# Performance work log

Hardware: AMD Instinct MI355X
Metric: run time of the kernel (lower is better)

## Reference

```python
import jax, jax.numpy as jnp
import numpy as np
import math

B, LQ, LK, D = 8, 4096, 32768, 64
LKS = min(8000, LK)                                    # sampled key window (K[:, :8000])
UPART = min(5 * LQ * int(np.ceil(np.log1p(LKS))), LKS)  # = 8000


def setup_inputs() -> dict:
    key = jax.random.key(0)
    k1, k2, k3, k4 = jax.random.split(key, 4)
    q = jax.random.normal(k1, (B, LQ, D), dtype=jnp.float32)
    K = jax.random.normal(k2, (B, LK, D), dtype=jnp.float32)
    V = jax.random.normal(k3, (B, LK, D), dtype=jnp.float32)
    index_sample = jax.random.randint(k4, (UPART,), 0, LKS)  # torch.randint(0, L_K, (U_part,))
    return {"q": q, "K": K, "V": V, "index_sample": index_sample}


def reference(q, K, V, index_sample):
    L_K = min(8000, K.shape[1])            # K_sample = K[:, :8000]; L_K = K_sample.size(1)
    L_Q = q.shape[1]
    d_k = q.shape[-1]
    log_L_Q = int(np.ceil(np.log1p(L_Q)))
    u = min(5 * log_L_Q, L_Q)

    # gather sampled keys (indices < 8000, indexing full K as in the source)
    K_samp = K[:, index_sample, :]                         # [B, U_part, D]
    QKs = jnp.einsum('bqd,bud->bqu', q, K_samp)            # [B, L_Q, U_part]
    # sparsity measure: max - mean (divided by L_K as in torch.div(sum, L_K))
    M = QKs.max(axis=-1) - QKs.sum(axis=-1) / L_K          # [B, L_Q]
    # torch topk(largest=False) -> smallest u values of M
    _, M_top = jax.lax.top_k(-M, u)                        # [B, u]
    Q_reduce = jnp.take_along_axis(q, M_top[:, :, None], axis=1)  # [B, u, D]

    attn_scores = jnp.einsum('bud,bkd->buk', Q_reduce, K) / math.sqrt(d_k)  # [B, u, L_K_full]
    attn_probs = jax.nn.softmax(attn_scores, axis=-1)
    attn_output = jnp.einsum('buk,bkd->bud', attn_probs, V)                  # [B, u, D]
    return attn_output, attn_scores
```

## Files before the change

kernel.cpp:

```cpp
#include <hip/hip_runtime.h>

#define BB 8
#define LQ 4096
#define LK 32768
#define DD 64
#define UU 8000
#define NU 45
#define TQ2 128
#define TUC 160
#define NCH (UU/TUC)
#define CHB (TUC*DD*2)
#define KT5 512
#define NT5 64

typedef short short8 __attribute__((ext_vector_type(8)));
typedef float floatx16 __attribute__((ext_vector_type(16)));

__device__ __forceinline__ float bf2f(unsigned short h){ return __uint_as_float(((unsigned int)h) << 16); }
__device__ __forceinline__ unsigned short f2bf(float f){
  unsigned int u = __float_as_uint(f);
  u += 0x7FFFu + ((u >> 16) & 1u);
  return (unsigned short)(u >> 16);
}
__device__ __forceinline__ unsigned int fkey(float v){
  unsigned int u = __float_as_uint(v);
  return (u & 0x80000000u) ? ~u : (u | 0x80000000u);
}

__global__ __launch_bounds__(256) void k_gather(const float* __restrict__ Kg, const int* __restrict__ idx,
                                                unsigned short* __restrict__ khi, unsigned short* __restrict__ kmid){
  const int b = blockIdx.y;
  const int row = blockIdx.x*32 + (threadIdx.x >> 3);
  const int oct = threadIdx.x & 7;
  const float* src = Kg + ((size_t)(b*LK + idx[row]))*DD + oct*8;
  float x[8];
  #pragma unroll
  for (int j=0;j<8;j++) x[j] = src[j];
  unsigned short h[8], m[8];
  #pragma unroll
  for (int j=0;j<8;j++){
    h[j] = f2bf(x[j]);
    m[j] = f2bf(x[j] - bf2f(h[j]));
  }
  const int osl = oct ^ (row & 7);
  size_t o = ((size_t)(b*UU + row))*DD + osl*8;
  #pragma unroll
  for (int j=0;j<8;j++){ khi[o+j]=h[j]; kmid[o+j]=m[j]; }
}

__global__ __launch_bounds__(64) void k_spart(const float* __restrict__ Kg, const int* __restrict__ idx,
                                              float* __restrict__ Spart){
  const int g = blockIdx.x, b = blockIdx.y, d = threadIdx.x;
  float acc = 0.0f;
  for (int j=0;j<64;j++){
    int u = g*64 + j;
    acc += Kg[((size_t)(b*LK + idx[u]))*DD + d];
  }
  Spart[((size_t)(b*125 + g))*DD + d] = acc;
}
__global__ __launch_bounds__(64) void k_sred(const float* __restrict__ Spart, float* __restrict__ Sb){
  const int b = blockIdx.x, d = threadIdx.x;
  float acc = 0.0f;
  for (int g=0; g<125; g++) acc += Spart[((size_t)(b*125 + g))*DD + d];
  Sb[b*DD + d] = acc;
}

__device__ __forceinline__ void stage_chunk(const char* gh, const char* gm,
                                            unsigned short* Bhb, unsigned short* Bmb,
                                            int w, int lane){
  #pragma unroll
  for (int i=0;i<5;i++){
    const int u = w*5 + i;
    if (u < 20){
      __builtin_amdgcn_global_load_lds(
        (const __attribute__((address_space(1))) void*)(gh + u*1024 + lane*16),
        (__attribute__((address_space(3))) void*)((char*)Bhb + u*1024 + lane*16),
        16, 0, 0);
    } else {
      __builtin_amdgcn_global_load_lds(
        (const __attribute__((address_space(1))) void*)(gm + (u-20)*1024 + lane*16),
        (__attribute__((address_space(3))) void*)((char*)Bmb + (u-20)*1024 + lane*16),
        16, 0, 0);
    }
  }
}

__global__ __launch_bounds__(512,2) void k_Mm(const float* __restrict__ q,
                                              const unsigned short* __restrict__ khi,
                                              const unsigned short* __restrict__ kmid,
                                              float* __restrict__ amaxG, int* __restrict__ acargG){
  const int wg = blockIdx.x;
  const int b = wg & 7, qt = wg >> 3;
  const int tid = threadIdx.x;
  const int w = tid >> 6, lane = tid & 63;
  const int tr = w & 3, sp = w >> 2;
  const int l31 = lane & 31, lh = lane >> 5;
  __shared__ __align__(16) unsigned short Bh[2][TUC*DD];
  __shared__ __align__(16) unsigned short Bm[2][TUC*DD];
  __shared__ float combV[TQ2][2];
  __shared__ int   combC[TQ2][2];

  const int qrow = qt*TQ2 + tr*32 + l31;
  short8 ahi[4], amid[4];
  {
    const float* qp = q + ((size_t)(b*LQ) + qrow)*DD;
    #pragma unroll
    for (int s=0;s<4;s++){
      const int d0 = s*16 + lh*8;
      float4 x0 = *(const float4*)(qp + d0);
      float4 x1 = *(const float4*)(qp + d0 + 4);
      float xs[8] = {x0.x,x0.y,x0.z,x0.w,x1.x,x1.y,x1.z,x1.w};
      short8 h, m;
      #pragma unroll
      for (int j=0;j<8;j++){
        unsigned short hb = f2bf(xs[j]);
        unsigned short mb = f2bf(xs[j] - bf2f(hb));
        h[j] = (short)hb; m[j] = (short)mb;
      }
      ahi[s]=h; amid[s]=m;
    }
  }

  float vmax[16]; int carg[16];
  #pragma unroll
  for (int r=0;r<16;r++){ vmax[r]=-INFINITY; carg[r]=0; }

  const size_t kbyte = (size_t)b*UU*DD*2;
  const char* ghbase = (const char*)khi + kbyte;
  const char* gmbase = (const char*)kmid + kbyte;

  stage_chunk(ghbase, gmbase, &Bh[0][0], &Bm[0][0], w, lane);
  int cur = 0;

  for (int c=0;c<NCH;c++){
    __syncthreads();
    if (c+1 < NCH){
      stage_chunk(ghbase + (size_t)(c+1)*CHB, gmbase + (size_t)(c+1)*CHB,
                  &Bh[cur^1][0], &Bm[cur^1][0], w, lane);
    }
    float lmax[16];
    #pragma unroll
    for (int r=0;r<16;r++) lmax[r] = -INFINITY;
    for (int t = ((c ^ sp) & 1); t < 5; t += 2){
      floatx16 accA = {0.f,0.f,0.f,0.f,0.f,0.f,0.f,0.f,0.f,0.f,0.f,0.f,0.f,0.f,0.f,0.f};
      floatx16 accB = {0.f,0.f,0.f,0.f,0.f,0.f,0.f,0.f,0.f,0.f,0.f,0.f,0.f,0.f,0.f,0.f};
      #pragma unroll
      for (int s=0;s<4;s++){
        const int eo = (t*32 + l31)*DD + (((s*2 + lh) ^ (l31 & 7))*8);
        short8 bh = *(const short8*)(&Bh[cur][eo]);
        short8 bm = *(const short8*)(&Bm[cur][eo]);
        if (s & 1){
          accB = __builtin_amdgcn_mfma_f32_32x32x16_bf16(amid[s], bh, accB, 0, 0, 0);
          accB = __builtin_amdgcn_mfma_f32_32x32x16_bf16(ahi[s],  bm, accB, 0, 0, 0);
          accB = __builtin_amdgcn_mfma_f32_32x32x16_bf16(ahi[s],  bh, accB, 0, 0, 0);
        } else {
          accA = __builtin_amdgcn_mfma_f32_32x32x16_bf16(amid[s], bh, accA, 0, 0, 0);
          accA = __builtin_amdgcn_mfma_f32_32x32x16_bf16(ahi[s],  bm, accA, 0, 0, 0);
          accA = __builtin_amdgcn_mfma_f32_32x32x16_bf16(ahi[s],  bh, accA, 0, 0, 0);
        }
      }
      #pragma unroll
      for (int r=0;r<16;r++) lmax[r] = fmaxf(lmax[r], accA[r] + accB[r]);
    }
    #pragma unroll
    for (int r=0;r<16;r++){
      if (lmax[r] > vmax[r]){ vmax[r] = lmax[r]; carg[r] = c; }
    }
    cur ^= 1;
  }
  #pragma unroll
  for (int st=1; st<32; st<<=1){
    #pragma unroll
    for (int r=0;r<16;r++){
      float ov = __shfl_xor(vmax[r], st);
      int   oc = __shfl_xor(carg[r], st);
      if (ov > vmax[r]){ vmax[r]=ov; carg[r]=oc; }
    }
  }
  if (l31 == 0){
    #pragma unroll
    for (int r=0;r<16;r++){
      int m = (r&3) + 8*(r>>2) + 4*lh;
      int ql = tr*32 + m;
      combV[ql][sp] = vmax[r];
      combC[ql][sp] = carg[r];
    }
  }
  __syncthreads();
  if (tid < TQ2){
    float v0 = combV[tid][0], v1 = combV[tid][1];
    int   c0 = combC[tid][0], c1 = combC[tid][1];
    bool t1 = v1 > v0;
    amaxG[(size_t)b*LQ + qt*TQ2 + tid] = t1 ? v1 : v0;
    acargG[(size_t)b*LQ + qt*TQ2 + tid] = t1 ? c1 : c0;
  }
}

__global__ __launch_bounds__(256) void k_bucket(const int* __restrict__ acargG,
                                                int* __restrict__ qlist, int* __restrict__ bstart){
  const int b = blockIdx.x, tid = threadIdx.x;
  __shared__ int cnt[NCH];
  __shared__ int pos[NCH];
  if (tid < NCH) cnt[tid] = 0;
  __syncthreads();
  for (int qq = tid; qq < LQ; qq += 256){
    int ch = acargG[(size_t)b*LQ + qq];
    ch = (ch < 0) ? 0 : ((ch >= NCH) ? NCH-1 : ch);
    atomicAdd(&cnt[ch], 1);
  }
  __syncthreads();
  if (tid == 0){
    int acc = 0;
    for (int c=0;c<NCH;c++){ pos[c] = acc; bstart[b*64 + c] = acc; acc += cnt[c]; }
    bstart[b*64 + NCH] = acc;
  }
  __syncthreads();
  for (int qq = tid; qq < LQ; qq += 256){
    int ch = acargG[(size_t)b*LQ + qq];
    ch = (ch < 0) ? 0 : ((ch >= NCH) ? NCH-1 : ch);
    int p = atomicAdd(&pos[ch], 1);
    p = (p < 0) ? 0 : ((p >= LQ) ? LQ-1 : p);
    qlist[(size_t)b*LQ + p] = qq;
  }
}

__global__ __launch_bounds__(256,3) void k_refb(const float* __restrict__ q, const float* __restrict__ Kg,
                                                const int* __restrict__ idx, const float* __restrict__ Sb,
                                                const int* __restrict__ qlist, const int* __restrict__ bstart,
                                                float* __restrict__ M){
  const int wg = blockIdx.x;
  const int b = wg & 7;
  const int r0 = wg >> 3;
  const int ch = r0 >> 2, part = r0 & 3;
  const int tid = threadIdx.x;
  const int w = tid >> 6, lane = tid & 63;
  const int quad = lane & 3, rg = lane >> 2;
  __shared__ __align__(16) float Kl[TUC*DD];
  float4* Kl4 = (float4*)Kl;
  for (int g = tid; g < TUC*16; g += 256){
    int row = g >> 4, s = g & 15;
    int gidx = idx[ch*TUC + row];
    float4 v = *(const float4*)(Kg + ((size_t)(b*LK + gidx))*DD + s*4);
    Kl4[row*16 + (s ^ (row & 7))] = v;
  }
  __syncthreads();

  const float4* sp4 = (const float4*)(Sb + b*DD + quad*16);
  const float4 S0 = sp4[0], S1 = sp4[1], S2 = sp4[2], S3 = sp4[3];
  const int sl0 = ((quad<<2)|0) ^ (rg & 7);
  const int sl1 = ((quad<<2)|1) ^ (rg & 7);
  const int sl2 = ((quad<<2)|2) ^ (rg & 7);
  const int sl3 = ((quad<<2)|3) ^ (rg & 7);
  const int rbs = rg*16;
  const int s0 = bstart[b*64 + ch], s1 = bstart[b*64 + ch + 1];
  const int gw = part*4 + w;

  for (int i = s0 + (gw<<1); i < s1; i += 32){
    const int qa = qlist[(size_t)b*LQ + i];
    const int i2 = (i+1 < s1) ? i+1 : i;
    const int qb = qlist[(size_t)b*LQ + i2];
    const float4* ap = (const float4*)(q + ((size_t)(b*LQ + qa))*DD + quad*16);
    const float4* bp = (const float4*)(q + ((size_t)(b*LQ + qb))*DD + quad*16);
    const float4 A0 = ap[0], A1 = ap[1], A2 = ap[2], A3 = ap[3];
    const float4 B0 = bp[0], B1 = bp[1], B2 = bp[2], B3 = bp[3];
    float mxa = -INFINITY, mxb = -INFINITY;
    #pragma unroll
    for (int p=0;p<10;p++){
      const int base = p*256 + rbs;
      float4 k0 = Kl4[base + sl0];
      float4 k1 = Kl4[base + sl1];
      float4 k2 = Kl4[base + sl2];
      float4 k3 = Kl4[base + sl3];
      float a0 = A0.x*k0.x, a1 = A0.y*k0.y, a2 = A0.z*k0.z, a3 = A0.w*k0.w;
      a0 = fmaf(A1.x,k1.x,a0); a1 = fmaf(A1.y,k1.y,a1); a2 = fmaf(A1.z,k1.z,a2); a3 = fmaf(A1.w,k1.w,a3);
      a0 = fmaf(A2.x,k2.x,a0); a1 = fmaf(A2.y,k2.y,a1); a2 = fmaf(A2.z,k2.z,a2); a3 = fmaf(A2.w,k2.w,a3);
      a0 = fmaf(A3.x,k3.x,a0); a1 = fmaf(A3.y,k3.y,a1); a2 = fmaf(A3.z,k3.z,a2); a3 = fmaf(A3.w,k3.w,a3);
      float c0 = B0.x*k0.x, c1 = B0.y*k0.y, c2 = B0.z*k0.z, c3 = B0.w*k0.w;
      c0 = fmaf(B1.x,k1.x,c0); c1 = fmaf(B1.y,k1.y,c1); c2 = fmaf(B1.z,k1.z,c2); c3 = fmaf(B1.w,k1.w,c3);
      c0 = fmaf(B2.x,k2.x,c0); c1 = fmaf(B2.y,k2.y,c1); c2 = fmaf(B2.z,k2.z,c2); c3 = fmaf(B2.w,k2.w,c3);
      c0 = fmaf(B3.x,k3.x,c0); c1 = fmaf(B3.y,k3.y,c1); c2 = fmaf(B3.z,k3.z,c2); c3 = fmaf(B3.w,k3.w,c3);
      float sa = (a0+a1)+(a2+a3);
      float sc = (c0+c1)+(c2+c3);
      sa += __shfl_xor(sa, 1);
      sa += __shfl_xor(sa, 2);
      sc += __shfl_xor(sc, 1);
      sc += __shfl_xor(sc, 2);
      mxa = fmaxf(mxa, sa);
      mxb = fmaxf(mxb, sc);
    }
    #pragma unroll
    for (int st=4; st<64; st<<=1){
      mxa = fmaxf(mxa, __shfl_xor(mxa, st));
      mxb = fmaxf(mxb, __shfl_xor(mxb, st));
    }
    float m0 = A0.x*S0.x, m1 = A0.y*S0.y, m2 = A0.z*S0.z, m3 = A0.w*S0.w;
    m0 = fmaf(A1.x,S1.x,m0); m1 = fmaf(A1.y,S1.y,m1); m2 = fmaf(A1.z,S1.z,m2); m3 = fmaf(A1.w,S1.w,m3);
    m0 = fmaf(A2.x,S2.x,m0); m1 = fmaf(A2.y,S2.y,m1); m2 = fmaf(A2.z,S2.z,m2); m3 = fmaf(A2.w,S2.w,m3);
    m0 = fmaf(A3.x,S3.x,m0); m1 = fmaf(A3.y,S3.y,m1); m2 = fmaf(A3.z,S3.z,m2); m3 = fmaf(A3.w,S3.w,m3);
    float msa = (m0+m1)+(m2+m3);
    msa += __shfl_xor(msa, 1);
    msa += __shfl_xor(msa, 2);
    float n0 = B0.x*S0.x, n1 = B0.y*S0.y, n2 = B0.z*S0.z, n3 = B0.w*S0.w;
    n0 = fmaf(B1.x,S1.x,n0); n1 = fmaf(B1.y,S1.y,n1); n2 = fmaf(B1.z,S1.z,n2); n3 = fmaf(B1.w,S1.w,n3);
    n0 = fmaf(B2.x,S2.x,n0); n1 = fmaf(B2.y,S2.y,n1); n2 = fmaf(B2.z,S2.z,n2); n3 = fmaf(B2.w,S2.w,n3);
    n0 = fmaf(B3.x,S3.x,n0); n1 = fmaf(B3.y,S3.y,n1); n2 = fmaf(B3.z,S3.z,n2); n3 = fmaf(B3.w,S3.w,n3);
    float msb = (n0+n1)+(n2+n3);
    msb += __shfl_xor(msb, 1);
    msb += __shfl_xor(msb, 2);
    if (lane == 0){
      M[(size_t)b*LQ + qa] = mxa - msa * (1.0f/8000.0f);
      if (i2 != i) M[(size_t)b*LQ + qb] = mxb - msb * (1.0f/8000.0f);
    }
  }
}

__global__ __launch_bounds__(256) void k_select(const float* __restrict__ Mg,
                                                const float* __restrict__ q,
                                                int* __restrict__ MtopG, float* __restrict__ Qred){
  const int b = blockIdx.x, tid = threadIdx.x;
  __shared__ float Mv[LQ];
  __shared__ unsigned long long wmin[4];
  __shared__ int mtop[NU];
  __shared__ int selB;
  for (int qq = tid; qq < LQ; qq += 256) Mv[qq] = Mg[(size_t)b*LQ + qq];
  __syncthreads();
  unsigned long long lm = ~0ull;
  #pragma unroll
  for (int i=0;i<16;i++){
    int qq = tid + 256*i;
    unsigned long long kk = (((unsigned long long)fkey(Mv[qq]))<<32) | (unsigned int)qq;
    lm = (kk < lm) ? kk : lm;
  }
  for (int i=0;i<NU;i++){
    unsigned long long v = lm;
    #pragma unroll
    for (int st=1; st<64; st<<=1){
      unsigned long long o = __shfl_xor(v, st);
      v = (o < v) ? o : v;
    }
    if ((tid & 63) == 0) wmin[tid>>6] = v;
    __syncthreads();
    if (tid == 0){
      unsigned long long g01 = (wmin[0] < wmin[1]) ? wmin[0] : wmin[1];
      unsigned long long g23 = (wmin[2] < wmin[3]) ? wmin[2] : wmin[3];
      unsigned long long g = (g01 < g23) ? g01 : g23;
      int sel = (int)(g & 0xFFFFFFFFull);
      mtop[i] = sel; selB = sel; Mv[sel] = INFINITY;
    }
    __syncthreads();
    int sel = selB;
    if (tid == (sel & 255)){
      unsigned long long nl = ~0ull;
      #pragma unroll
      for (int j=0;j<16;j++){
        int qq = tid + 256*j;
        unsigned long long kk = (((unsigned long long)fkey(Mv[qq]))<<32) | (unsigned int)qq;
        nl = (kk < nl) ? kk : nl;
      }
      lm = nl;
    }
    __syncthreads();
  }
  if (tid < NU) MtopG[b*NU + tid] = mtop[tid];
  for (int e = tid; e < NU*DD; e += 256){
    int ui = e >> 6, d = e & 63;
    Qred[((size_t)(b*NU + ui))*DD + d] = q[((size_t)(b*LQ + mtop[ui]))*DD + d];
  }
}

#define QFMA(i) { float4 p = qr4[i]; \
  a0 = fmaf(kv##i.x, p.x, a0); a1 = fmaf(kv##i.y, p.y, a1); \
  a2 = fmaf(kv##i.z, p.z, a2); a3 = fmaf(kv##i.w, p.w, a3); }

__global__ __launch_bounds__(256) void k_scores(const float* __restrict__ Kg,
                                                const float* __restrict__ Qred,
                                                float* __restrict__ out1,
                                                float* __restrict__ pm, float* __restrict__ pl){
  const int b = blockIdx.y;
  const int k = blockIdx.x*256 + threadIdx.x;
  const int lane = threadIdx.x & 63, w = threadIdx.x >> 6;
  const int pi = blockIdx.x*4 + w;
  const float4* kp4 = (const float4*)(Kg + ((size_t)(b*LK + k))*DD);
  const float4 kv0  = kp4[0],  kv1  = kp4[1],  kv2  = kp4[2],  kv3  = kp4[3];
  const float4 kv4  = kp4[4],  kv5  = kp4[5],  kv6  = kp4[6],  kv7  = kp4[7];
  const float4 kv8  = kp4[8],  kv9  = kp4[9],  kv10 = kp4[10], kv11 = kp4[11];
  const float4 kv12 = kp4[12], kv13 = kp4[13], kv14 = kp4[14], kv15 = kp4[15];
  for (int u=0; u<NU; u++){
    const float4* qr4 = (const float4*)(Qred + ((size_t)(b*NU+u))*DD);
    float a0 = 0.f, a1 = 0.f, a2 = 0.f, a3 = 0.f;
    QFMA(0)  QFMA(1)  QFMA(2)  QFMA(3)
    QFMA(4)  QFMA(5)  QFMA(6)  QFMA(7)
    QFMA(8)  QFMA(9)  QFMA(10) QFMA(11)
    QFMA(12) QFMA(13) QFMA(14) QFMA(15)
    float s = ((a0+a1)+(a2+a3)) * 0.125f;
    out1[((size_t)(b*NU+u)<<15) + k] = s;
    float mw = s;
    #pragma unroll
    for (int st=1; st<64; st<<=1) mw = fmaxf(mw, __shfl_xor(mw, st));
    float e = __expf(s - mw);
    #pragma unroll
    for (int st=1; st<64; st<<=1) e += __shfl_xor(e, st);
    if (lane == 0){
      size_t r = (size_t)(b*NU + u);
      pm[r*512 + pi] = mw;
      pl[r*512 + pi] = e;
    }
  }
}

__global__ __launch_bounds__(256) void k_rowred(const float* __restrict__ pm, const float* __restrict__ pl,
                                                float* __restrict__ rowm, float* __restrict__ rowinvl){
  const int r = blockIdx.x, tid = threadIdx.x;
  __shared__ float red[256];
  float m = -INFINITY;
  for (int i = tid; i < 512; i += 256) m = fmaxf(m, pm[(size_t)r*512 + i]);
  red[tid] = m; __syncthreads();
  for (int s=128;s>0;s>>=1){ if (tid<s) red[tid] = fmaxf(red[tid], red[tid+s]); __syncthreads(); }
  m = red[0]; __syncthreads();
  float sm = 0.0f;
  for (int i = tid; i < 512; i += 256)
    sm += pl[(size_t)r*512 + i] * __expf(pm[(size_t)r*512 + i] - m);
  red[tid] = sm; __syncthreads();
  for (int s=128;s>0;s>>=1){ if (tid<s) red[tid] += red[tid+s]; __syncthreads(); }
  if (tid==0){ rowm[r] = m; rowinvl[r] = 1.0f/red[0]; }
}

__global__ __launch_bounds__(512) void k_pv(const float* __restrict__ Vg,
                                            const float* __restrict__ out1,
                                            const float* __restrict__ rowm, const float* __restrict__ rowinvl,
                                            float* __restrict__ pvpart){
  const int kt = blockIdx.x, b = blockIdx.y, tid = threadIdx.x;
  const int lane = tid & 63, w = tid >> 6;
  const int u0 = w*6;
  __shared__ float Vl[128][65];
  __shared__ __align__(16) float Pl[48][132];
  float acc[6];
  #pragma unroll
  for (int j=0;j<6;j++) acc[j] = 0.0f;
  for (int sc=0; sc<4; sc++){
    const int k0 = kt*KT5 + sc*128;
    {
      int r = tid >> 2, h = tid & 3;
      const float* vp = Vg + ((size_t)(b*LK + k0 + r))*DD + h*16;
      #pragma unroll
      for (int j=0;j<4;j++){
        float4 t = ((const float4*)vp)[j];
        Vl[r][h*16 + 4*j]   = t.x;
        Vl[r][h*16 + 4*j+1] = t.y;
        Vl[r][h*16 + 4*j+2] = t.z;
        Vl[r][h*16 + 4*j+3] = t.w;
      }
    }
    for (int e = tid; e < 48*128; e += 512){
      int u = e >> 7, kk = e & 127;
      float p = 0.0f;
      if (u < NU){
        int r = b*NU + u;
        float s = out1[((size_t)r<<15) + k0 + kk];
        p = __expf(s - rowm[r]) * rowinvl[r];
      }
      Pl[u][kk] = p;
    }
    __syncthreads();
    for (int kk4=0; kk4<32; kk4++){
      float v0 = Vl[4*kk4+0][lane];
      float v1 = Vl[4*kk4+1][lane];
      float v2 = Vl[4*kk4+2][lane];
      float v3 = Vl[4*kk4+3][lane];
      #pragma unroll
      for (int j=0;j<6;j++){
        float4 p = *reinterpret_cast<const float4*>(&Pl[u0+j][4*kk4]);
        acc[j] = fmaf(p.w, v3, fmaf(p.z, v2, fmaf(p.y, v1, fmaf(p.x, v0, acc[j]))));
      }
    }
    __syncthreads();
  }
  #pragma unroll
  for (int j=0;j<6;j++){
    if (u0 + j < NU){
      pvpart[(((size_t)(b*NU + u0 + j))*NT5 + kt)*DD + lane] = acc[j];
    }
  }
}

__global__ __launch_bounds__(256) void k_final(const float* __restrict__ pvpart, float* __restrict__ out0){
  int e = blockIdx.x*256 + threadIdx.x;
  if (e >= BB*NU*DD) return;
  int d = e & 63; int r = e >> 6;
  float s = 0.0f;
  for (int t=0;t<NT5;t++) s += pvpart[((size_t)r*NT5 + t)*DD + d];
  out0[e] = s;
}

extern "C" void kernel_launch(void* const* d_in, const int* in_sizes, int n_in,
                              void* d_out, int out_size, void* d_ws, size_t ws_size,
                              hipStream_t stream){
  const float* q  = (const float*)d_in[0];
  const float* K  = (const float*)d_in[1];
  const float* V  = (const float*)d_in[2];
  const int* idx  = (const int*)d_in[3];
  float* out0 = (float*)d_out;
  float* out1 = out0 + BB*NU*DD;

  float* ws = (float*)d_ws;
  unsigned short* khi  = (unsigned short*)ws;
  float*  pvpart = ws;
  unsigned short* kmid = (unsigned short*)(ws + (size_t)BB*UU*DD/2);
  float* pm      = ws + (size_t)BB*UU*DD/2;
  float* pl      = pm + (size_t)BB*NU*512;
  float* Spart   = ws + (size_t)BB*UU*DD;
  float* Sb      = Spart + 64000;
  float* amax    = Sb + 512;
  int*   acarg   = (int*)(amax + BB*LQ);
  float* Mbq     = (float*)(acarg + BB*LQ);
  float* Qred    = Mbq + BB*LQ;
  float* rowm    = Qred + (size_t)BB*NU*DD;
  float* rowinvl = rowm + 512;
  int*   Mtop    = (int*)(rowinvl + 512);
  int*   qlist   = Mtop + 512;
  int*   bstart  = qlist + (size_t)BB*LQ;

  k_gather<<<dim3(UU/32, BB), 256, 0, stream>>>(K, idx, khi, kmid);
  k_spart<<<dim3(125, BB), 64, 0, stream>>>(K, idx, Spart);
  k_sred<<<BB, 64, 0, stream>>>(Spart, Sb);
  k_Mm<<<(LQ/TQ2)*BB, 512, 0, stream>>>(q, khi, kmid, amax, acarg);
  k_bucket<<<BB, 256, 0, stream>>>(acarg, qlist, bstart);
  k_refb<<<NCH*4*BB, 256, 0, stream>>>(q, K, idx, Sb, qlist, bstart, Mbq);
  k_select<<<BB, 256, 0, stream>>>(Mbq, q, Mtop, Qred);
  k_scores<<<dim3(LK/256, BB), 256, 0, stream>>>(K, Qred, out1, pm, pl);
  k_rowred<<<BB*NU, 256, 0, stream>>>(pm, pl, rowm, rowinvl);
  k_pv<<<dim3(NT5, BB), 512, 0, stream>>>(V, out1, rowm, rowinvl, pvpart);
  k_final<<<(BB*NU*DD + 255)/256, 256, 0, stream>>>(pvpart, out0);
}
```

Measured before the change: 523.5 us.

## Split k_Mm key chunks across two parity workgroups to double grid size

Each k_Mm workgroup now processes only even or odd key chunks, doubling the grid from 256 to 512 workgroups. Per-parity partial max/argmax results are written to a doubled buffer and merged in k_bucket, which also caches the chosen chunk in shared memory instead of reloading it. The combine scratch now reuses the staging LDS to save shared memory. The aim is better CU occupancy on a grid that was too small for the device, at the cost of reloading and converting q twice and a little extra merge work.

```diff
diff --git a/kernel.cpp b/kernel.cpp
--- a/kernel.cpp
+++ b/kernel.cpp
@@ -88,17 +88,15 @@
 __global__ __launch_bounds__(512,2) void k_Mm(const float* __restrict__ q,
                                               const unsigned short* __restrict__ khi,
                                               const unsigned short* __restrict__ kmid,
-                                              float* __restrict__ amaxG, int* __restrict__ acargG){
+                                              float* __restrict__ amax2, int* __restrict__ acarg2){
   const int wg = blockIdx.x;
-  const int b = wg & 7, qt = wg >> 3;
+  const int b = wg & 7, par = (wg >> 3) & 1, qt = wg >> 4;
   const int tid = threadIdx.x;
   const int w = tid >> 6, lane = tid & 63;
   const int tr = w & 3, sp = w >> 2;
   const int l31 = lane & 31, lh = lane >> 5;
   __shared__ __align__(16) unsigned short Bh[2][TUC*DD];
   __shared__ __align__(16) unsigned short Bm[2][TUC*DD];
-  __shared__ float combV[TQ2][2];
-  __shared__ int   combC[TQ2][2];
 
   const int qrow = qt*TQ2 + tr*32 + l31;
   short8 ahi[4], amid[4];
@@ -129,19 +127,20 @@
   const char* ghbase = (const char*)khi + kbyte;
   const char* gmbase = (const char*)kmid + kbyte;
 
-  stage_chunk(ghbase, gmbase, &Bh[0][0], &Bm[0][0], w, lane);
+  stage_chunk(ghbase + (size_t)par*CHB, gmbase + (size_t)par*CHB, &Bh[0][0], &Bm[0][0], w, lane);
   int cur = 0;
-
-  for (int c=0;c<NCH;c++){
+  int it = 0;
+
+  for (int c = par; c < NCH; c += 2, it++){
     __syncthreads();
-    if (c+1 < NCH){
-      stage_chunk(ghbase + (size_t)(c+1)*CHB, gmbase + (size_t)(c+1)*CHB,
+    if (c+2 < NCH){
+      stage_chunk(ghbase + (size_t)(c+2)*CHB, gmbase + (size_t)(c+2)*CHB,
                   &Bh[cur^1][0], &Bm[cur^1][0], w, lane);
     }
     float lmax[16];
     #pragma unroll
     for (int r=0;r<16;r++) lmax[r] = -INFINITY;
-    for (int t = ((c ^ sp) & 1); t < 5; t += 2){
+    for (int t = ((it ^ sp) & 1); t < 5; t += 2){
       floatx16 accA = {0.f,0.f,0.f,0.f,0.f,0.f,0.f,0.f,0.f,0.f,0.f,0.f,0.f,0.f,0.f,0.f};
       floatx16 accB = {0.f,0.f,0.f,0.f,0.f,0.f,0.f,0.f,0.f,0.f,0.f,0.f,0.f,0.f,0.f,0.f};
       #pragma unroll
@@ -177,35 +176,46 @@
       if (ov > vmax[r]){ vmax[r]=ov; carg[r]=oc; }
     }
   }
+  __syncthreads();
+  float* combV = (float*)&Bh[0][0];
+  int*   combC = (int*)(combV + TQ2*2);
   if (l31 == 0){
     #pragma unroll
     for (int r=0;r<16;r++){
       int m = (r&3) + 8*(r>>2) + 4*lh;
       int ql = tr*32 + m;
-      combV[ql][sp] = vmax[r];
-      combC[ql][sp] = carg[r];
+      combV[ql*2 + sp] = vmax[r];
+      combC[ql*2 + sp] = carg[r];
     }
   }
   __syncthreads();
   if (tid < TQ2){
-    float v0 = combV[tid][0], v1 = combV[tid][1];
-    int   c0 = combC[tid][0], c1 = combC[tid][1];
+    float v0 = combV[tid*2+0], v1 = combV[tid*2+1];
+    int   c0 = combC[tid*2+0], c1 = combC[tid*2+1];
     bool t1 = v1 > v0;
-    amaxG[(size_t)b*LQ + qt*TQ2 + tid] = t1 ? v1 : v0;
-    acargG[(size_t)b*LQ + qt*TQ2 + tid] = t1 ? c1 : c0;
-  }
-}
-
-__global__ __launch_bounds__(256) void k_bucket(const int* __restrict__ acargG,
+    size_t o = ((size_t)(par*BB + b))*LQ + qt*TQ2 + tid;
+    amax2[o]  = t1 ? v1 : v0;
+    acarg2[o] = t1 ? c1 : c0;
+  }
+}
+
+__global__ __launch_bounds__(256) void k_bucket(const float* __restrict__ amax2,
+                                                const int* __restrict__ acarg2,
                                                 int* __restrict__ qlist, int* __restrict__ bstart){
   const int b = blockIdx.x, tid = threadIdx.x;
+  __shared__ unsigned char chs[LQ];
   __shared__ int cnt[NCH];
   __shared__ int pos[NCH];
   if (tid < NCH) cnt[tid] = 0;
   __syncthreads();
   for (int qq = tid; qq < LQ; qq += 256){
-    int ch = acargG[(size_t)b*LQ + qq];
+    float v0 = amax2[((size_t)b)*LQ + qq];
+    float v1 = amax2[((size_t)(BB + b))*LQ + qq];
+    int   c0 = acarg2[((size_t)b)*LQ + qq];
+    int   c1 = acarg2[((size_t)(BB + b))*LQ + qq];
+    int ch = (v1 > v0 || (v1 == v0 && c1 < c0)) ? c1 : c0;
     ch = (ch < 0) ? 0 : ((ch >= NCH) ? NCH-1 : ch);
+    chs[qq] = (unsigned char)ch;
     atomicAdd(&cnt[ch], 1);
   }
   __syncthreads();
@@ -216,8 +226,7 @@
   }
   __syncthreads();
   for (int qq = tid; qq < LQ; qq += 256){
-    int ch = acargG[(size_t)b*LQ + qq];
-    ch = (ch < 0) ? 0 : ((ch >= NCH) ? NCH-1 : ch);
+    int ch = chs[qq];
     int p = atomicAdd(&pos[ch], 1);
     p = (p < 0) ? 0 : ((p >= LQ) ? LQ-1 : p);
     qlist[(size_t)b*LQ + p] = qq;
@@ -510,9 +519,9 @@
   float* pl      = pm + (size_t)BB*NU*512;
   float* Spart   = ws + (size_t)BB*UU*DD;
   float* Sb      = Spart + 64000;
-  float* amax    = Sb + 512;
-  int*   acarg   = (int*)(amax + BB*LQ);
-  float* Mbq     = (float*)(acarg + BB*LQ);
+  float* amax2   = Sb + 512;
+  int*   acarg2  = (int*)(amax2 + 2*(size_t)BB*LQ);
+  float* Mbq     = (float*)(acarg2 + 2*(size_t)BB*LQ);
   float* Qred    = Mbq + BB*LQ;
   float* rowm    = Qred + (size_t)BB*NU*DD;
   float* rowinvl = rowm + 512;
@@ -523,8 +532,8 @@
   k_gather<<<dim3(UU/32, BB), 256, 0, stream>>>(K, idx, khi, kmid);
   k_spart<<<dim3(125, BB), 64, 0, stream>>>(K, idx, Spart);
   k_sred<<<BB, 64, 0, stream>>>(Spart, Sb);
-  k_Mm<<<(LQ/TQ2)*BB, 512, 0, stream>>>(q, khi, kmid, amax, acarg);
-  k_bucket<<<BB, 256, 0, stream>>>(acarg, qlist, bstart);
+  k_Mm<<<(LQ/TQ2)*2*BB, 512, 0, stream>>>(q, khi, kmid, amax2, acarg2);
+  k_bucket<<<BB, 256, 0, stream>>>(amax2, acarg2, qlist, bstart);
   k_refb<<<NCH*4*BB, 256, 0, stream>>>(q, K, idx, Sb, qlist, bstart, Mbq);
   k_select<<<BB, 256, 0, stream>>>(Mbq, q, Mtop, Qred);
   k_scores<<<dim3(LK/256, BB), 256, 0, stream>>>(K, Qred, out1, pm, pl);
```

Result: no change. 526.0 us (+0.5%).
